# Performance work log

Measured on AMD Instinct MI355X. Metric: run time of the kernel, lower is better.

## Reference

```python
import jax, jax.numpy as jnp
import numpy as np

B, T, C = 4, 2048, 1024
H = 16
HD = C // H

def setup_inputs() -> dict:
    key = jax.random.key(0)
    k1, k2, k3 = jax.random.split(key, 3)
    x = jax.random.normal(k1, (B, T, C), dtype=jnp.float32)
    w_attn = jax.random.normal(k2, (C, 3 * C), dtype=jnp.float32) * 0.02
    b_attn = jnp.zeros((3 * C,), dtype=jnp.float32)
    w_proj = jax.random.normal(k3, (C, C), dtype=jnp.float32) * 0.02
    b_proj = jnp.zeros((C,), dtype=jnp.float32)
    return {"x": x, "w_attn": w_attn, "b_attn": b_attn, "w_proj": w_proj, "b_proj": b_proj}

def reference(x, w_attn, b_attn, w_proj, b_proj):
    Bx, Tx, Cx = x.shape
    qkv = x @ w_attn + b_attn                      # [B,T,3C]
    q, k, v = jnp.split(qkv, 3, axis=-1)
    # [B,T,C] -> [B,H,T,HD]
    q = q.reshape(Bx, Tx, H, HD).transpose(0, 2, 1, 3)
    k = k.reshape(Bx, Tx, H, HD).transpose(0, 2, 1, 3)
    v = v.reshape(Bx, Tx, H, HD).transpose(0, 2, 1, 3)
    scale = 1.0 / jnp.sqrt(jnp.asarray(HD, dtype=x.dtype))
    att = jnp.einsum('bhqd,bhkd->bhqk', q, k) * scale
    causal = jnp.tril(jnp.ones((Tx, Tx), dtype=bool))
    att = jnp.where(causal[None, None], att, jnp.finfo(att.dtype).min)
    att = jax.nn.softmax(att, axis=-1)
    y = jnp.einsum('bhqk,bhkd->bhqd', att, v)       # [B,H,T,HD]
    y = y.transpose(0, 2, 1, 3).reshape(Bx, Tx, Cx)
    return y @ w_proj + b_proj
```

## Files before the change

### kernel.cpp

```cpp
#include <hip/hip_runtime.h>
#include <hip/hip_bf16.h>

#define B_ 4
#define T_ 2048
#define C_ 1024
#define H_ 16
#define HD_ 64
#define BT_ (B_*T_)
#define C3_ (3*C_)
#define BHTD_ ((size_t)B_*H_*T_*HD_)

#define QSCALE 0.18033688011112042f

using u16 = unsigned short;
using u32 = unsigned int;
using bf16x8 = __attribute__((ext_vector_type(8))) short;
using f32x4  = __attribute__((ext_vector_type(4))) float;
using f32x16 = __attribute__((ext_vector_type(16))) float;
using u16x4  = __attribute__((ext_vector_type(4))) u16;
typedef int i32x2 __attribute__((ext_vector_type(2)));

#if __has_builtin(__builtin_amdgcn_exp2f)
#define EXP2(x) __builtin_amdgcn_exp2f(x)
#else
#define EXP2(x) exp2f(x)
#endif

__device__ __forceinline__ u16 f2bf(float f) {
  u32 u = __float_as_uint(f);
  u += 0x7fffu + ((u >> 16) & 1u);
  return (u16)(u >> 16);
}

__device__ __forceinline__ u32 cvtpk(float lo, float hi) {
  u32 r;
  asm("v_cvt_pk_bf16_f32 %0, %1, %2" : "=v"(r) : "v"(lo), "v"(hi));
  return r;
}

__device__ __forceinline__ void plswap(u32 &a, u32 &b) {
#if __has_builtin(__builtin_amdgcn_permlane32_swap)
  i32x2 r = __builtin_amdgcn_permlane32_swap((int)a, (int)b, false, false);
  a = (u32)r[0]; b = (u32)r[1];
#else
  asm volatile("v_permlane32_swap_b32 %0, %1" : "+v"(a), "+v"(b));
#endif
}

__device__ __forceinline__ float xmaxf(float x) {
  u32 a = __float_as_uint(x), b = a;
  plswap(a, b);
  return fmaxf(__uint_as_float(a), __uint_as_float(b));
}
__device__ __forceinline__ float xaddf(float x) {
  u32 a = __float_as_uint(x), b = a;
  plswap(a, b);
  return __uint_as_float(a) + __uint_as_float(b);
}

__device__ __forceinline__ void gload16(const void* g,
                                        __attribute__((address_space(3))) void* l) {
  __builtin_amdgcn_global_load_lds((const __attribute__((address_space(1))) void*)g,
                                   l, 16, 0, 0);
}

__global__ __launch_bounds__(256) void k_cvt_bf16(const float* __restrict__ in,
                                                  u16* __restrict__ out) {
  size_t i = (size_t)(blockIdx.x * blockDim.x + threadIdx.x) * 4;
  f32x4 f = *(const f32x4*)(in + i);
  u16x4 o;
  o[0] = f2bf(f[0]); o[1] = f2bf(f[1]); o[2] = f2bf(f[2]); o[3] = f2bf(f[3]);
  *(u16x4*)(out + i) = o;
}

__global__ __launch_bounds__(256) void k_transpose_bf16(const float* __restrict__ w,
                                                        u16* __restrict__ wt,
                                                        int K, int N) {
  __shared__ float t[32][33];
  int n0 = blockIdx.x * 32, k0 = blockIdx.y * 32;
  int tx = threadIdx.x & 31;
  int ty = threadIdx.x >> 5;
  #pragma unroll
  for (int r = 0; r < 4; ++r)
    t[ty + r*8][tx] = w[(size_t)(k0 + ty + r*8) * N + n0 + tx];
  __syncthreads();
  #pragma unroll
  for (int r = 0; r < 4; ++r)
    wt[(size_t)(n0 + ty + r*8) * K + k0 + tx] = f2bf(t[tx][ty + r*8]);
}

__global__ __launch_bounds__(256) void k_transpose_v(const u16* __restrict__ src,
                                                     u16* __restrict__ dst) {
  __shared__ u16 t[64][72];
  int bh = blockIdx.y;
  int t0 = blockIdx.x * 64;
  const u16* s = src + (size_t)bh * T_ * HD_;
  u16* d = dst + (size_t)bh * HD_ * T_;
  int r = threadIdx.x >> 2, c0 = (threadIdx.x & 3) * 16;
  bf16x8 a0 = *(const bf16x8*)(s + (size_t)(t0 + r)*HD_ + c0);
  bf16x8 a1 = *(const bf16x8*)(s + (size_t)(t0 + r)*HD_ + c0 + 8);
  #pragma unroll
  for (int j = 0; j < 8; ++j) t[r][c0 + j] = (u16)a0[j];
  #pragma unroll
  for (int j = 0; j < 8; ++j) t[r][c0 + 8 + j] = (u16)a1[j];
  __syncthreads();
  bf16x8 b0, b1;
  #pragma unroll
  for (int j = 0; j < 8; ++j) b0[j] = (short)t[c0 + j][r];
  #pragma unroll
  for (int j = 0; j < 8; ++j) b1[j] = (short)t[c0 + 8 + j][r];
  *(bf16x8*)(d + (size_t)r*T_ + t0 + c0) = b0;
  *(bf16x8*)(d + (size_t)r*T_ + t0 + c0 + 8) = b1;
}

template<int EPI>
__global__ __launch_bounds__(256) void k_gemm(const u16* __restrict__ A,
                                              const u16* __restrict__ Bt,
                                              const float* __restrict__ bias,
                                              void* __restrict__ outp,
                                              void* __restrict__ outp2,
                                              int K) {
  __shared__ __align__(16) u16 lA[128*32];
  __shared__ __align__(16) u16 lB[128*32];
  int tid = threadIdx.x;
  int wave = tid >> 6, lane = tid & 63;
  int wr = wave >> 1, wc = wave & 1;
  int lrow = lane & 15, lgrp = lane >> 4;
  int nwg = gridDim.x * gridDim.y;
  int bidf = blockIdx.y * gridDim.x + blockIdx.x;
  int swzb = (bidf & 7) * (nwg >> 3) + (bidf >> 3);
  int bx = swzb % gridDim.x, by = swzb / gridDim.x;
  int row0 = by * 128, col0 = bx * 128;

  f32x4 zero = {0.f, 0.f, 0.f, 0.f};
  f32x4 acc[4][4];
  #pragma unroll
  for (int m = 0; m < 4; ++m)
    #pragma unroll
    for (int n = 0; n < 4; ++n) acc[m][n] = zero;

  for (int kt = 0; kt < K; kt += 32) {
    #pragma unroll
    for (int p = 0; p < 2; ++p) {
      int c = (wave*2 + p)*64 + lane;
      int r = c >> 2, kc = c & 3;
      int sk = kc ^ ((r >> 1) & 3);
      gload16(A  + (size_t)(row0 + r)*K + kt + sk*8,
              (__attribute__((address_space(3))) char*)lA + (wave*2 + p)*1024);
      gload16(Bt + (size_t)(col0 + r)*K + kt + sk*8,
              (__attribute__((address_space(3))) char*)lB + (wave*2 + p)*1024);
    }
    __syncthreads();
    bf16x8 af[4], bfr[4];
    #pragma unroll
    for (int m = 0; m < 4; ++m) {
      int row = wr*64 + m*16 + lrow;
      af[m] = *(const bf16x8*)(lA + row*32 + (lgrp ^ ((row >> 1) & 3))*8);
    }
    #pragma unroll
    for (int n = 0; n < 4; ++n) {
      int row = wc*64 + n*16 + lrow;
      bfr[n] = *(const bf16x8*)(lB + row*32 + (lgrp ^ ((row >> 1) & 3))*8);
    }
    #pragma unroll
    for (int m = 0; m < 4; ++m)
      #pragma unroll
      for (int n = 0; n < 4; ++n)
        acc[m][n] = __builtin_amdgcn_mfma_f32_16x16x32_bf16(af[m], bfr[n], acc[m][n], 0, 0, 0);
    __syncthreads();
  }

  #pragma unroll
  for (int m = 0; m < 4; ++m) {
    #pragma unroll
    for (int n = 0; n < 4; ++n) {
      int gcol = col0 + wc*64 + n*16 + lrow;
      float bv = bias[gcol];
      #pragma unroll
      for (int r = 0; r < 4; ++r) {
        int grow = row0 + wr*64 + m*16 + lgrp*4 + r;
        float val = acc[m][n][r] + bv;
        if (EPI == 0) {
          int which = gcol >> 10, c = gcol & 1023;
          int hh = c >> 6, d = c & 63;
          int bb = grow >> 11, tt = grow & 2047;
          if (which == 0) val *= QSCALE;
          size_t idx = ((size_t)(bb*H_ + hh)*T_ + tt)*HD_ + d;
          if (which == 2)
            ((u16*)outp2)[idx] = f2bf(val);
          else
            ((u16*)outp)[(size_t)which*BHTD_ + idx] = f2bf(val);
        } else {
          ((float*)outp)[(size_t)grow*C_ + gcol] = val;
        }
      }
    }
  }
}

__global__ __launch_bounds__(256, 2) void k_attn(const u16* __restrict__ q,
                                                 const u16* __restrict__ k,
                                                 const u16* __restrict__ vt,
                                                 u16* __restrict__ y) {
  __shared__ __align__(16) u16 Kl[2][64][72];
  __shared__ __align__(16) u16 Vl[2][64][72];
  int tid = threadIdx.x;
  int wave = tid >> 6, lane = tid & 63;
  int l31 = lane & 31, hi = lane >> 5;
  int bid = blockIdx.x;
  int head = bid & 63;
  int jA = bid >> 6;
  int bidx = head >> 4, hh = head & 15;
  const u16* qb = q  + (size_t)head * T_ * HD_;
  const u16* kb = k  + (size_t)head * T_ * HD_;
  const u16* vb = vt + (size_t)head * HD_ * T_;

  int sr = tid >> 2;
  int sc = (tid & 3) * 16;

  f32x16 zero16 = {0.f,0.f,0.f,0.f,0.f,0.f,0.f,0.f,0.f,0.f,0.f,0.f,0.f,0.f,0.f,0.f};

  auto runqt = [&](int j) {
    int qr0 = j*128 + wave*32;
    bf16x8 qf[4];
    {
      const u16* qrow = qb + (size_t)(qr0 + l31)*HD_ + hi*8;
      #pragma unroll
      for (int i = 0; i < 4; ++i) qf[i] = *(const bf16x8*)(qrow + 16*i);
    }
    f32x16 od0 = zero16, od1 = zero16;
    float mrun = -1e30f, lrun = 0.f;
    int qg = qr0 + l31;
    int nt = 2*j + 2;

    {
      const u16* ks = kb + (size_t)sr*HD_ + sc;
      const u16* vs = vb + (size_t)sr*T_ + sc;
      bf16x8 k0 = *(const bf16x8*)ks, k1 = *(const bf16x8*)(ks + 8);
      bf16x8 v0 = *(const bf16x8*)vs, v1 = *(const bf16x8*)(vs + 8);
      *(bf16x8*)&Kl[0][sr][sc] = k0; *(bf16x8*)&Kl[0][sr][sc + 8] = k1;
      *(bf16x8*)&Vl[0][sr][sc] = v0; *(bf16x8*)&Vl[0][sr][sc + 8] = v1;
      __syncthreads();
    }

    for (int t = 0; t < nt; ++t) {
      int kv0 = t*64;
      int cb = t & 1, nb = cb ^ 1;
      bool haveNext = (t + 1 < nt);

      bf16x8 nk0, nk1, nv0, nv1;
      if (haveNext) {
        const u16* ks = kb + (size_t)(kv0 + 64 + sr)*HD_ + sc;
        const u16* vs = vb + (size_t)sr*T_ + (kv0 + 64) + sc;
        nk0 = *(const bf16x8*)ks; nk1 = *(const bf16x8*)(ks + 8);
        nv0 = *(const bf16x8*)vs; nv1 = *(const bf16x8*)(vs + 8);
      }

      if (kv0 <= qr0 + 31) {
        bf16x8 kf[8], vf[8];
        #pragma unroll
        for (int i = 0; i < 4; ++i) {
          int cc = 16*i + 8*hi;
          kf[i]     = *(const bf16x8*)&Kl[cb][l31][cc];
          kf[4 + i] = *(const bf16x8*)&Kl[cb][l31 + 32][cc];
          vf[i]     = *(const bf16x8*)&Vl[cb][l31][cc];
          vf[4 + i] = *(const bf16x8*)&Vl[cb][l31 + 32][cc];
        }

        f32x16 s0 = zero16, s1 = zero16;
        __builtin_amdgcn_s_setprio(1);
        s0 = __builtin_amdgcn_mfma_f32_32x32x16_bf16(kf[0], qf[0], s0, 0, 0, 0);
        s1 = __builtin_amdgcn_mfma_f32_32x32x16_bf16(kf[4], qf[0], s1, 0, 0, 0);
        s0 = __builtin_amdgcn_mfma_f32_32x32x16_bf16(kf[1], qf[1], s0, 0, 0, 0);
        s1 = __builtin_amdgcn_mfma_f32_32x32x16_bf16(kf[5], qf[1], s1, 0, 0, 0);
        s0 = __builtin_amdgcn_mfma_f32_32x32x16_bf16(kf[2], qf[2], s0, 0, 0, 0);
        s1 = __builtin_amdgcn_mfma_f32_32x32x16_bf16(kf[6], qf[2], s1, 0, 0, 0);
        s0 = __builtin_amdgcn_mfma_f32_32x32x16_bf16(kf[3], qf[3], s0, 0, 0, 0);
        s1 = __builtin_amdgcn_mfma_f32_32x32x16_bf16(kf[7], qf[3], s1, 0, 0, 0);
        __builtin_amdgcn_s_setprio(0);

        if (kv0 + 63 > qr0) {
          #pragma unroll
          for (int r = 0; r < 16; ++r) {
            int kl2 = (r & 3) + 8*(r >> 2) + 4*hi;
            if (kv0 + kl2      > qg) s0[r] = -1e30f;
            if (kv0 + 32 + kl2 > qg) s1[r] = -1e30f;
          }
        }

        float tmx[16];
        #pragma unroll
        for (int i = 0; i < 16; ++i) tmx[i] = fmaxf(s0[i], s1[i]);
        #pragma unroll
        for (int off = 8; off > 0; off >>= 1)
          #pragma unroll
          for (int i = 0; i < 8; ++i)
            if (i < off) tmx[i] = fmaxf(tmx[i], tmx[i + off]);
        float pmax = xmaxf(tmx[0]);

        if (!__all(pmax <= mrun)) {
          float mnew = fmaxf(mrun, pmax);
          float ex = EXP2(mrun - mnew);
          mrun = mnew;
          lrun *= ex;
          #pragma unroll
          for (int i = 0; i < 16; ++i) { od0[i] *= ex; od1[i] *= ex; }
        }

        #pragma unroll
        for (int i = 0; i < 16; ++i) s0[i] = EXP2(s0[i] - mrun);
        #pragma unroll
        for (int i = 0; i < 16; ++i) s1[i] = EXP2(s1[i] - mrun);
        float u[16];
        #pragma unroll
        for (int i = 0; i < 16; ++i) u[i] = s0[i] + s1[i];
        #pragma unroll
        for (int off = 8; off > 0; off >>= 1)
          #pragma unroll
          for (int i = 0; i < 8; ++i)
            if (i < off) u[i] = u[i] + u[i + off];
        lrun += xaddf(u[0]);

        bf16x8 pf0, pf1, pf2, pf3;
        {
          u32 a0 = cvtpk(s0[0], s0[1]),   a1 = cvtpk(s0[2], s0[3]);
          u32 b0 = cvtpk(s0[4], s0[5]),   b1 = cvtpk(s0[6], s0[7]);
          plswap(a0, b0); plswap(a1, b1);
          u32 wa[4] = {a0, a1, b0, b1};
          __builtin_memcpy(&pf0, wa, 16);
        }
        {
          u32 a0 = cvtpk(s0[8], s0[9]),   a1 = cvtpk(s0[10], s0[11]);
          u32 b0 = cvtpk(s0[12], s0[13]), b1 = cvtpk(s0[14], s0[15]);
          plswap(a0, b0); plswap(a1, b1);
          u32 wa[4] = {a0, a1, b0, b1};
          __builtin_memcpy(&pf1, wa, 16);
        }
        {
          u32 a0 = cvtpk(s1[0], s1[1]),   a1 = cvtpk(s1[2], s1[3]);
          u32 b0 = cvtpk(s1[4], s1[5]),   b1 = cvtpk(s1[6], s1[7]);
          plswap(a0, b0); plswap(a1, b1);
          u32 wa[4] = {a0, a1, b0, b1};
          __builtin_memcpy(&pf2, wa, 16);
        }
        {
          u32 a0 = cvtpk(s1[8], s1[9]),   a1 = cvtpk(s1[10], s1[11]);
          u32 b0 = cvtpk(s1[12], s1[13]), b1 = cvtpk(s1[14], s1[15]);
          plswap(a0, b0); plswap(a1, b1);
          u32 wa[4] = {a0, a1, b0, b1};
          __builtin_memcpy(&pf3, wa, 16);
        }

        __builtin_amdgcn_s_setprio(1);
        od0 = __builtin_amdgcn_mfma_f32_32x32x16_bf16(vf[0], pf0, od0, 0, 0, 0);
        od0 = __builtin_amdgcn_mfma_f32_32x32x16_bf16(vf[1], pf1, od0, 0, 0, 0);
        od0 = __builtin_amdgcn_mfma_f32_32x32x16_bf16(vf[2], pf2, od0, 0, 0, 0);
        od0 = __builtin_amdgcn_mfma_f32_32x32x16_bf16(vf[3], pf3, od0, 0, 0, 0);
        od1 = __builtin_amdgcn_mfma_f32_32x32x16_bf16(vf[4], pf0, od1, 0, 0, 0);
        od1 = __builtin_amdgcn_mfma_f32_32x32x16_bf16(vf[5], pf1, od1, 0, 0, 0);
        od1 = __builtin_amdgcn_mfma_f32_32x32x16_bf16(vf[6], pf2, od1, 0, 0, 0);
        od1 = __builtin_amdgcn_mfma_f32_32x32x16_bf16(vf[7], pf3, od1, 0, 0, 0);
        __builtin_amdgcn_s_setprio(0);
      }

      if (haveNext) {
        *(bf16x8*)&Kl[nb][sr][sc] = nk0; *(bf16x8*)&Kl[nb][sr][sc + 8] = nk1;
        *(bf16x8*)&Vl[nb][sr][sc] = nv0; *(bf16x8*)&Vl[nb][sr][sc + 8] = nv1;
      }
      __syncthreads();
    }

    float inv = 1.0f / lrun;
    u16* yrow = y + ((size_t)(bidx*T_) + qr0 + l31)*C_ + hh*64;
    #pragma unroll
    for (int r = 0; r < 8; ++r) {
      int dp = ((2*r) & 3) + 8*(r >> 1) + 4*hi;
      *(u32*)(yrow + dp)      = cvtpk(od0[2*r]*inv, od0[2*r+1]*inv);
      *(u32*)(yrow + 32 + dp) = cvtpk(od1[2*r]*inv, od1[2*r+1]*inv);
    }
  };

  runqt(jA);
  runqt(15 - jA);
}

extern "C" void kernel_launch(void* const* d_in, const int* in_sizes, int n_in,
                              void* d_out, int out_size, void* d_ws, size_t ws_size,
                              hipStream_t stream) {
  const float* x      = (const float*)d_in[0];
  const float* w_attn = (const float*)d_in[1];
  const float* b_attn = (const float*)d_in[2];
  const float* w_proj = (const float*)d_in[3];
  const float* b_proj = (const float*)d_in[4];

  char* ws = (char*)d_ws;
  size_t off = 0;
  auto walloc = [&](size_t bytes) -> void* {
    void* p = ws + off;
    off += (bytes + 255) & ~(size_t)255;
    return p;
  };
  u16* xbf  = (u16*)walloc((size_t)BT_ * C_ * 2);
  u16* wat  = (u16*)walloc((size_t)C3_ * C_ * 2);
  u16* wpt  = (u16*)walloc((size_t)C_ * C_ * 2);
  u16* qkv  = (u16*)walloc(3 * BHTD_ * 2);
  u16* vtmp = (u16*)walloc(BHTD_ * 2);
  u16* qp = qkv;
  u16* kp = qkv + BHTD_;
  u16* vp = qkv + 2*BHTD_;
  u16* ybf = xbf;

  k_cvt_bf16<<<(BT_*C_)/1024, 256, 0, stream>>>(x, xbf);
  k_transpose_bf16<<<dim3(C3_/32, C_/32), 256, 0, stream>>>(w_attn, wat, C_, C3_);
  k_transpose_bf16<<<dim3(C_/32, C_/32), 256, 0, stream>>>(w_proj, wpt, C_, C_);
  k_gemm<0><<<dim3(C3_/128, BT_/128), 256, 0, stream>>>(xbf, wat, b_attn, (void*)qkv, (void*)vtmp, C_);
  k_transpose_v<<<dim3(T_/64, B_*H_), 256, 0, stream>>>(vtmp, vp);
  k_attn<<<dim3(512), 256, 0, stream>>>(qp, kp, vp, ybf);
  k_gemm<1><<<dim3(C_/128, BT_/128), 256, 0, stream>>>(ybf, wpt, b_proj, d_out, nullptr, C_);
}
```

Measured before the change: 185.8 us.

## Store QKV row-major and double GEMM K-tile to 64

The QKV GEMM epilogue now writes a plain row-major [B*T, 3C] bf16 buffer instead of scattering into per-head [B,H,T,HD] layouts. The attention and V-transpose kernels read Q, K and V with a 3C row stride. Separately, the GEMM K-step grows from 32 to 64 with an 8-way XOR swizzle, halving the number of barriers per tile at the cost of more LDS per block. The simpler epilogue gives more contiguous stores, while attention loads become strided across rows.

```diff
diff --git a/kernel.cpp b/kernel.cpp
--- a/kernel.cpp
+++ b/kernel.cpp
@@ -89,16 +89,17 @@
     wt[(size_t)(n0 + ty + r*8) * K + k0 + tx] = f2bf(t[tx][ty + r*8]);
 }
 
-__global__ __launch_bounds__(256) void k_transpose_v(const u16* __restrict__ src,
+__global__ __launch_bounds__(256) void k_transpose_v(const u16* __restrict__ qkv3,
                                                      u16* __restrict__ dst) {
   __shared__ u16 t[64][72];
   int bh = blockIdx.y;
+  int bb = bh >> 4, hh = bh & 15;
   int t0 = blockIdx.x * 64;
-  const u16* s = src + (size_t)bh * T_ * HD_;
+  const u16* s = qkv3 + (size_t)(bb*T_)*C3_ + 2*C_ + hh*64;
   u16* d = dst + (size_t)bh * HD_ * T_;
   int r = threadIdx.x >> 2, c0 = (threadIdx.x & 3) * 16;
-  bf16x8 a0 = *(const bf16x8*)(s + (size_t)(t0 + r)*HD_ + c0);
-  bf16x8 a1 = *(const bf16x8*)(s + (size_t)(t0 + r)*HD_ + c0 + 8);
+  bf16x8 a0 = *(const bf16x8*)(s + (size_t)(t0 + r)*C3_ + c0);
+  bf16x8 a1 = *(const bf16x8*)(s + (size_t)(t0 + r)*C3_ + c0 + 8);
   #pragma unroll
   for (int j = 0; j < 8; ++j) t[r][c0 + j] = (u16)a0[j];
   #pragma unroll
@@ -118,10 +119,9 @@
                                               const u16* __restrict__ Bt,
                                               const float* __restrict__ bias,
                                               void* __restrict__ outp,
-                                              void* __restrict__ outp2,
                                               int K) {
-  __shared__ __align__(16) u16 lA[128*32];
-  __shared__ __align__(16) u16 lB[128*32];
+  __shared__ __align__(16) u16 lA[128*64];
+  __shared__ __align__(16) u16 lB[128*64];
   int tid = threadIdx.x;
   int wave = tid >> 6, lane = tid & 63;
   int wr = wave >> 1, wc = wave & 1;
@@ -139,34 +139,37 @@
     #pragma unroll
     for (int n = 0; n < 4; ++n) acc[m][n] = zero;
 
-  for (int kt = 0; kt < K; kt += 32) {
+  for (int kt = 0; kt < K; kt += 64) {
     #pragma unroll
-    for (int p = 0; p < 2; ++p) {
-      int c = (wave*2 + p)*64 + lane;
-      int r = c >> 2, kc = c & 3;
-      int sk = kc ^ ((r >> 1) & 3);
+    for (int it = 0; it < 4; ++it) {
+      int c = tid + it*256;
+      int r = c >> 3, sl = c & 7;
+      int sk = sl ^ (r & 7);
       gload16(A  + (size_t)(row0 + r)*K + kt + sk*8,
-              (__attribute__((address_space(3))) char*)lA + (wave*2 + p)*1024);
+              (__attribute__((address_space(3))) char*)lA + it*4096 + wave*1024);
       gload16(Bt + (size_t)(col0 + r)*K + kt + sk*8,
-              (__attribute__((address_space(3))) char*)lB + (wave*2 + p)*1024);
+              (__attribute__((address_space(3))) char*)lB + it*4096 + wave*1024);
     }
     __syncthreads();
-    bf16x8 af[4], bfr[4];
     #pragma unroll
-    for (int m = 0; m < 4; ++m) {
-      int row = wr*64 + m*16 + lrow;
-      af[m] = *(const bf16x8*)(lA + row*32 + (lgrp ^ ((row >> 1) & 3))*8);
-    }
-    #pragma unroll
-    for (int n = 0; n < 4; ++n) {
-      int row = wc*64 + n*16 + lrow;
-      bfr[n] = *(const bf16x8*)(lB + row*32 + (lgrp ^ ((row >> 1) & 3))*8);
-    }
-    #pragma unroll
-    for (int m = 0; m < 4; ++m)
+    for (int kk = 0; kk < 2; ++kk) {
+      bf16x8 af[4], bfr[4];
       #pragma unroll
-      for (int n = 0; n < 4; ++n)
-        acc[m][n] = __builtin_amdgcn_mfma_f32_16x16x32_bf16(af[m], bfr[n], acc[m][n], 0, 0, 0);
+      for (int m = 0; m < 4; ++m) {
+        int row = wr*64 + m*16 + lrow;
+        af[m] = *(const bf16x8*)(lA + row*64 + (((kk*4 + lgrp) ^ (row & 7)))*8);
+      }
+      #pragma unroll
+      for (int n = 0; n < 4; ++n) {
+        int row = wc*64 + n*16 + lrow;
+        bfr[n] = *(const bf16x8*)(lB + row*64 + (((kk*4 + lgrp) ^ (row & 7)))*8);
+      }
+      #pragma unroll
+      for (int m = 0; m < 4; ++m)
+        #pragma unroll
+        for (int n = 0; n < 4; ++n)
+          acc[m][n] = __builtin_amdgcn_mfma_f32_16x16x32_bf16(af[m], bfr[n], acc[m][n], 0, 0, 0);
+    }
     __syncthreads();
   }
 
@@ -181,15 +184,8 @@
         int grow = row0 + wr*64 + m*16 + lgrp*4 + r;
         float val = acc[m][n][r] + bv;
         if (EPI == 0) {
-          int which = gcol >> 10, c = gcol & 1023;
-          int hh = c >> 6, d = c & 63;
-          int bb = grow >> 11, tt = grow & 2047;
-          if (which == 0) val *= QSCALE;
-          size_t idx = ((size_t)(bb*H_ + hh)*T_ + tt)*HD_ + d;
-          if (which == 2)
-            ((u16*)outp2)[idx] = f2bf(val);
-          else
-            ((u16*)outp)[(size_t)which*BHTD_ + idx] = f2bf(val);
+          if (gcol < C_) val *= QSCALE;
+          ((u16*)outp)[(size_t)grow*C3_ + gcol] = f2bf(val);
         } else {
           ((float*)outp)[(size_t)grow*C_ + gcol] = val;
         }
@@ -198,8 +194,7 @@
   }
 }
 
-__global__ __launch_bounds__(256, 2) void k_attn(const u16* __restrict__ q,
-                                                 const u16* __restrict__ k,
+__global__ __launch_bounds__(256, 2) void k_attn(const u16* __restrict__ qkv3,
                                                  const u16* __restrict__ vt,
                                                  u16* __restrict__ y) {
   __shared__ __align__(16) u16 Kl[2][64][72];
@@ -211,8 +206,8 @@
   int head = bid & 63;
   int jA = bid >> 6;
   int bidx = head >> 4, hh = head & 15;
-  const u16* qb = q  + (size_t)head * T_ * HD_;
-  const u16* kb = k  + (size_t)head * T_ * HD_;
+  const u16* qb = qkv3 + (size_t)(bidx*T_)*C3_ + hh*64;
+  const u16* kb = qkv3 + (size_t)(bidx*T_)*C3_ + C_ + hh*64;
   const u16* vb = vt + (size_t)head * HD_ * T_;
 
   int sr = tid >> 2;
@@ -224,7 +219,7 @@
     int qr0 = j*128 + wave*32;
     bf16x8 qf[4];
     {
-      const u16* qrow = qb + (size_t)(qr0 + l31)*HD_ + hi*8;
+      const u16* qrow = qb + (size_t)(qr0 + l31)*C3_ + hi*8;
       #pragma unroll
       for (int i = 0; i < 4; ++i) qf[i] = *(const bf16x8*)(qrow + 16*i);
     }
@@ -234,7 +229,7 @@
     int nt = 2*j + 2;
 
     {
-      const u16* ks = kb + (size_t)sr*HD_ + sc;
+      const u16* ks = kb + (size_t)sr*C3_ + sc;
       const u16* vs = vb + (size_t)sr*T_ + sc;
       bf16x8 k0 = *(const bf16x8*)ks, k1 = *(const bf16x8*)(ks + 8);
       bf16x8 v0 = *(const bf16x8*)vs, v1 = *(const bf16x8*)(vs + 8);
@@ -250,7 +245,7 @@
 
       bf16x8 nk0, nk1, nv0, nv1;
       if (haveNext) {
-        const u16* ks = kb + (size_t)(kv0 + 64 + sr)*HD_ + sc;
+        const u16* ks = kb + (size_t)(kv0 + 64 + sr)*C3_ + sc;
         const u16* vs = vb + (size_t)sr*T_ + (kv0 + 64) + sc;
         nk0 = *(const bf16x8*)ks; nk1 = *(const bf16x8*)(ks + 8);
         nv0 = *(const bf16x8*)vs; nv1 = *(const bf16x8*)(vs + 8);
@@ -403,18 +398,15 @@
   u16* xbf  = (u16*)walloc((size_t)BT_ * C_ * 2);
   u16* wat  = (u16*)walloc((size_t)C3_ * C_ * 2);
   u16* wpt  = (u16*)walloc((size_t)C_ * C_ * 2);
-  u16* qkv  = (u16*)walloc(3 * BHTD_ * 2);
-  u16* vtmp = (u16*)walloc(BHTD_ * 2);
-  u16* qp = qkv;
-  u16* kp = qkv + BHTD_;
-  u16* vp = qkv + 2*BHTD_;
+  u16* qkv3 = (u16*)walloc((size_t)BT_ * C3_ * 2);
+  u16* vT   = (u16*)walloc(BHTD_ * 2);
   u16* ybf = xbf;
 
   k_cvt_bf16<<<(BT_*C_)/1024, 256, 0, stream>>>(x, xbf);
   k_transpose_bf16<<<dim3(C3_/32, C_/32), 256, 0, stream>>>(w_attn, wat, C_, C3_);
   k_transpose_bf16<<<dim3(C_/32, C_/32), 256, 0, stream>>>(w_proj, wpt, C_, C_);
-  k_gemm<0><<<dim3(C3_/128, BT_/128), 256, 0, stream>>>(xbf, wat, b_attn, (void*)qkv, (void*)vtmp, C_);
-  k_transpose_v<<<dim3(T_/64, B_*H_), 256, 0, stream>>>(vtmp, vp);
-  k_attn<<<dim3(512), 256, 0, stream>>>(qp, kp, vp, ybf);
-  k_gemm<1><<<dim3(C_/128, BT_/128), 256, 0, stream>>>(ybf, wpt, b_proj, d_out, nullptr, C_);
-}
+  k_gemm<0><<<dim3(C3_/128, BT_/128), 256, 0, stream>>>(xbf, wat, b_attn, (void*)qkv3, C_);
+  k_transpose_v<<<dim3(T_/64, B_*H_), 256, 0, stream>>>(qkv3, vT);
+  k_attn<<<dim3(512), 256, 0, stream>>>(qkv3, vT, ybf);
+  k_gemm<1><<<dim3(C_/128, BT_/128), 256, 0, stream>>>(ybf, wpt, b_proj, d_out, C_);
+}
```

Result: faster. 181.1 us (-2.5%).
